# Kernel tuning notes

Hardware: AMD Instinct MI355X
Metric: run time of the kernel (lower is better)

Reference implementation:

```python
import math
import jax, jax.numpy as jnp
import numpy as np

D_MODEL, D_HEAD, N_HEADS, COND = 1024, 64, 16, 1024
BATCH, L_T, H_S, W_S = 2, 8, 16, 16
N_FREQS = D_HEAD // 8  # rotary freqs per axis; 3 axes -> rotates 3*D_HEAD/4 dims
EPS = 1e-6


def _ste(x, qx):
    # straight-through estimator: forward qx, backward identity
    return x + jax.lax.stop_gradient(qx - x)


def _weight_quant(w):
    # BitNet-1.58 ternary: per-tensor absmean scale, round to {-1,0,1}
    s = 1.0 / jnp.clip(jnp.mean(jnp.abs(w)), 1e-5)
    return jnp.clip(jnp.round(w * s), -1.0, 1.0) / s


def _act_quant(x):
    # per-token int8 absmax quant
    s = 127.0 / jnp.clip(jnp.max(jnp.abs(x), axis=-1, keepdims=True), 1e-5)
    return jnp.clip(jnp.round(x * s), -128.0, 127.0) / s


def bit_linear(x, w):
    return _ste(x, _act_quant(x)) @ _ste(w, _weight_quant(w)).T


def rms_norm(x, scale, eps=EPS):
    ms = jnp.mean(x * x, axis=-1, keepdims=True)
    return x * scale * jax.lax.rsqrt(ms + eps)


def apply_rotary_emb(x, theta):
    # rotate first 2*d dims of x (d = theta.shape[-1]); pass the rest through
    d = theta.shape[-1]
    x1, x2, x3 = x[..., :d], x[..., d:2 * d], x[..., 2 * d:]
    cos, sin = jnp.cos(theta), jnp.sin(theta)
    return jnp.concatenate([x1 * cos - x2 * sin, x2 * cos + x1 * sin, x3], axis=-1)


def make_freqs():
    # log-spaced pi..10*pi, distributed across heads (k-diffusion AxialRoPE init)
    log_min, log_max = math.log(math.pi), math.log(10.0 * math.pi)
    f = jnp.exp(jnp.linspace(log_min, log_max, N_HEADS * N_FREQS + 1)[:-1])
    return f.reshape(N_FREQS, N_HEADS).T.astype(jnp.float32)  # [n_heads, n_freqs]


def setup_inputs() -> dict:
    key = jax.random.key(0)
    ks = jax.random.split(key, 6)
    x = jax.random.normal(ks[0], (BATCH, L_T, H_S, W_S, D_MODEL), jnp.float32)
    pos = jax.random.uniform(ks[1], (BATCH, L_T, H_S, W_S, 3), jnp.float32) * 2.0 - 1.0
    cond = jax.random.normal(ks[2], (BATCH, COND), jnp.float32)
    norm_w = jax.random.normal(ks[3], (D_MODEL, COND), jnp.float32) * 0.02
    qkv_w = jax.random.normal(ks[4], (3 * D_MODEL, D_MODEL), jnp.float32) * 0.02
    out_w = jax.random.normal(ks[5], (D_MODEL, D_MODEL), jnp.float32) * 0.02
    scale = jnp.full((N_HEADS,), 10.0, jnp.float32)
    freqs = make_freqs()
    return dict(x=x, pos=pos, cond=cond, norm_w=norm_w, qkv_w=qkv_w,
                out_w=out_w, scale=scale, freqs=freqs)


def reference(x, pos, cond, norm_w, qkv_w, out_w, scale, freqs):
    n, l, h, w, d = x.shape
    L = l * h * w
    skip = x
    # AdaRMSNorm: scale = 1 + zero-init Linear(cond)
    ada = 1.0 + cond @ norm_w.T                      # [n, d]
    xn = rms_norm(x, ada[:, None, None, None, :])
    # BitLinear QKV projection
    qkv = bit_linear(xn.reshape(n, L, d), qkv_w)     # [n, L, 3d]
    qkv = qkv.reshape(n, L, 3, N_HEADS, D_HEAD).transpose(2, 0, 3, 1, 4)  # [3,n,nh,L,e]
    q, k, v = qkv[0], qkv[1], qkv[2]
    # cosine-sim rescale with learned per-head scale
    sqrt_s = jnp.sqrt(scale)[:, None, None]          # [nh,1,1]
    q = q * (sqrt_s * jax.lax.rsqrt(jnp.sum(q * q, -1, keepdims=True) + EPS))
    k = k * (sqrt_s * jax.lax.rsqrt(jnp.sum(k * k, -1, keepdims=True) + EPS))
    # axial RoPE over 3 axes
    p = pos.reshape(n, L, 3)
    theta = jnp.concatenate([p[..., None, a:a + 1] * freqs for a in range(3)], axis=-1)  # [n,L,nh,3*nf]
    theta = jnp.moveaxis(theta, -2, -3)              # [n,nh,L,3*nf]
    q = apply_rotary_emb(q, theta)
    k = apply_rotary_emb(k, theta)
    # SDPA with scale=1.0 (cosine-sim already scaled)
    attn = jax.nn.softmax(jnp.einsum('nhqe,nhke->nhqk', q, k), axis=-1)
    o = jnp.einsum('nhqk,nhke->nhqe', attn, v)       # [n,nh,L,e]
    o = o.transpose(0, 2, 1, 3).reshape(n, L, d)
    o = bit_linear(o, out_w).reshape(n, l, h, w, d)
    return o + skip
```

## Files before the change

kernel.cpp:

```cpp
#include <hip/hip_runtime.h>
#include <hip/hip_bf16.h>
#include <math.h>

typedef __attribute__((ext_vector_type(8))) short bf16x8;
typedef __attribute__((ext_vector_type(4))) short bf16x4;
typedef __attribute__((ext_vector_type(4))) float f32x4;
typedef __attribute__((ext_vector_type(16))) float f32x16;
typedef __attribute__((ext_vector_type(4))) unsigned u32x4;
typedef __attribute__((ext_vector_type(2))) unsigned u32x2;
typedef __attribute__((ext_vector_type(4))) int i32x4;

#define DEV static __device__ __forceinline__
#define LOG2E 1.4426950408889634f
#define INV2PI 0.15915494309189535f

DEV unsigned short f2bf(float f) {
  unsigned int u = __float_as_uint(f);
  u += 0x7FFFu + ((u >> 16) & 1u);
  return (unsigned short)(u >> 16);
}
DEV float bf2f(unsigned short h) { return __uint_as_float(((unsigned int)h) << 16); }
DEV unsigned cvtpk(float lo, float hi) {
  unsigned r;
  asm("v_cvt_pk_bf16_f32 %0, %1, %2" : "=v"(r) : "v"(lo), "v"(hi));
  return r;
}
DEV float exp2raw(float x) {
  float r;
  asm("v_exp_f32 %0, %1" : "=v"(r) : "v"(x));
  return r;
}
DEV float fract_raw(float x) { float r; asm("v_fract_f32 %0, %1" : "=v"(r) : "v"(x)); return r; }
DEV float sin_rev(float x)   { float r; asm("v_sin_f32 %0, %1"   : "=v"(r) : "v"(x)); return r; }
DEV float cos_rev(float x)   { float r; asm("v_cos_f32 %0, %1"   : "=v"(r) : "v"(x)); return r; }
DEV float wsum(float v) { for (int o = 32; o; o >>= 1) v += __shfl_xor(v, o); return v; }
DEV float wmaxr(float v) { for (int o = 32; o; o >>= 1) v = fmaxf(v, __shfl_xor(v, o)); return v; }

DEV void gload_lds16(const void* g, void* s) {
  __builtin_amdgcn_global_load_lds(
      (const __attribute__((address_space(1))) unsigned int*)g,
      (__attribute__((address_space(3))) unsigned int*)s, 16, 0, 0);
}

__global__ __launch_bounds__(256) void wrada_k(const float* __restrict__ qw,
                                               const float* __restrict__ ow,
                                               const float* __restrict__ cond,
                                               const float* __restrict__ nw,
                                               float* __restrict__ rowsum,
                                               float* __restrict__ ada) {
  if (blockIdx.x < 4096) {
    int row = blockIdx.x;
    const float* p = (row < 3072) ? (qw + (size_t)row * 1024)
                                  : (ow + (size_t)(row - 3072) * 1024);
    f32x4 v = *(const f32x4*)&p[threadIdx.x * 4];
    float s = fabsf(v[0]) + fabsf(v[1]) + fabsf(v[2]) + fabsf(v[3]);
    s = wsum(s);
    __shared__ float sh[4];
    if ((threadIdx.x & 63) == 0) sh[threadIdx.x >> 6] = s;
    __syncthreads();
    if (threadIdx.x == 0) rowsum[row] = sh[0] + sh[1] + sh[2] + sh[3];
  } else {
    int bid2 = blockIdx.x - 4096;
    int b = bid2 >> 8;
    int j = (bid2 & 255) * 4 + (threadIdx.x >> 6);
    int l = threadIdx.x & 63;
    const float* cp = cond + b * 1024;
    const float* wp = nw + (size_t)j * 1024;
    float s = 0.f;
    for (int c = l; c < 1024; c += 64) s += cp[c] * wp[c];
    s = wsum(s);
    if (l == 0) ada[b * 1024 + j] = 1.f + s;
  }
}

__global__ __launch_bounds__(256) void finalize_k(const float* __restrict__ rowsum,
                                                  float* __restrict__ scales) {
  float s1 = 0.f, s2 = 0.f;
  for (int i = threadIdx.x; i < 3072; i += 256) s1 += rowsum[i];
  for (int i = threadIdx.x; i < 1024; i += 256) s2 += rowsum[3072 + i];
  s1 = wsum(s1); s2 = wsum(s2);
  __shared__ float sh1[4], sh2[4];
  if ((threadIdx.x & 63) == 0) { sh1[threadIdx.x >> 6] = s1; sh2[threadIdx.x >> 6] = s2; }
  __syncthreads();
  if (threadIdx.x == 0) {
    float m1 = fmaxf((sh1[0] + sh1[1] + sh1[2] + sh1[3]) / (3072.f * 1024.f), 1e-5f);
    float m2 = fmaxf((sh2[0] + sh2[1] + sh2[2] + sh2[3]) / (1024.f * 1024.f), 1e-5f);
    scales[0] = m1; scales[1] = 1.f / m1;
    scales[2] = m2; scales[3] = 1.f / m2;
  }
}

__global__ __launch_bounds__(256) void wqrms_k(const float* __restrict__ qw,
                                               const float* __restrict__ ow,
                                               const float* __restrict__ scales,
                                               const float* __restrict__ x,
                                               const float* __restrict__ ada,
                                               signed char* __restrict__ Wq,
                                               signed char* __restrict__ Wo,
                                               signed char* __restrict__ Aq,
                                               float* __restrict__ ascale) {
  if (blockIdx.x < 4096) {
    int i0 = (blockIdx.x * 256 + threadIdx.x) * 4;
    if (i0 < 3072 * 1024) {
      f32x4 v = *(const f32x4*)&qw[i0];
      unsigned pk = 0;
      for (int j = 0; j < 4; j++) {
        int t = (int)fminf(fmaxf(rintf(v[j] * scales[1]), -1.f), 1.f);
        pk |= ((unsigned)t & 0xFFu) << (8 * j);
      }
      *(unsigned*)&Wq[i0] = pk;
    } else {
      int k = i0 - 3072 * 1024;
      f32x4 v = *(const f32x4*)&ow[k];
      unsigned pk = 0;
      for (int j = 0; j < 4; j++) {
        int t = (int)fminf(fmaxf(rintf(v[j] * scales[3]), -1.f), 1.f);
        pk |= ((unsigned)t & 0xFFu) << (8 * j);
      }
      *(unsigned*)&Wo[k] = pk;
    }
  } else {
    int row = blockIdx.x - 4096;
    int b = row >> 11;
    const float* xr = x + (size_t)row * 1024;
    const float* ar = ada + b * 1024;
    int t4 = threadIdx.x * 4;
    f32x4 v = *(const f32x4*)&xr[t4];
    float ss = v[0]*v[0] + v[1]*v[1] + v[2]*v[2] + v[3]*v[3];
    ss = wsum(ss);
    __shared__ float sh[4], sh2[4];
    if ((threadIdx.x & 63) == 0) sh[threadIdx.x >> 6] = ss;
    __syncthreads();
    float inv = rsqrtf((sh[0] + sh[1] + sh[2] + sh[3]) * (1.f / 1024.f) + 1e-6f);
    f32x4 a = *(const f32x4*)&ar[t4];
    float xn[4]; float mx = 0.f;
    for (int i = 0; i < 4; i++) { xn[i] = v[i] * a[i] * inv; mx = fmaxf(mx, fabsf(xn[i])); }
    mx = wmaxr(mx);
    if ((threadIdx.x & 63) == 0) sh2[threadIdx.x >> 6] = mx;
    __syncthreads();
    float rmax = fmaxf(fmaxf(sh2[0], sh2[1]), fmaxf(sh2[2], sh2[3]));
    float s = 127.f / fmaxf(rmax, 1e-5f);
    unsigned pk = 0;
    for (int i = 0; i < 4; i++) {
      int ai = (int)fminf(fmaxf(rintf(xn[i] * s), -128.f), 127.f);
      pk |= ((unsigned)ai & 0xFFu) << (8 * i);
    }
    *(unsigned*)&Aq[(size_t)row * 1024 + t4] = pk;
    if (threadIdx.x == 0) ascale[row] = 1.f / s;
  }
}

__global__ __launch_bounds__(256) void oquant_k(const unsigned short* __restrict__ Opart,
                                                const float* __restrict__ ms,
                                                signed char* __restrict__ Oq,
                                                float* __restrict__ oscale) {
  int row = blockIdx.x;
  int b = row >> 11, qrow = row & 2047;
  int t4 = threadIdx.x * 4;
  int h = t4 >> 6, e0 = t4 & 63;
  int bh = b * 16 + h;
  size_t i0 = (size_t)bh * 2048 + qrow;
  size_t i1 = (size_t)(32 + bh) * 2048 + qrow;
  float w = 1.f / (ms[i0] + ms[i1]);
  bf16x4 o0 = *(const bf16x4*)&Opart[i0 * 64 + e0];
  bf16x4 o1 = *(const bf16x4*)&Opart[i1 * 64 + e0];
  float v[4]; float mx = 0.f;
  for (int i = 0; i < 4; i++) {
    v[i] = (bf2f((unsigned short)o0[i]) + bf2f((unsigned short)o1[i])) * w;
    mx = fmaxf(mx, fabsf(v[i]));
  }
  mx = wmaxr(mx);
  __shared__ float sh[4];
  if ((threadIdx.x & 63) == 0) sh[threadIdx.x >> 6] = mx;
  __syncthreads();
  float rmax = fmaxf(fmaxf(sh[0], sh[1]), fmaxf(sh[2], sh[3]));
  float s = 127.f / fmaxf(rmax, 1e-5f);
  float is = 1.f / s;
  unsigned pk = 0;
  for (int i = 0; i < 4; i++) {
    int ai = (int)fminf(fmaxf(rintf(v[i] * s), -128.f), 127.f);
    pk |= ((unsigned)ai & 0xFFu) << (8 * i);
  }
  *(unsigned*)&Oq[(size_t)row * 1024 + t4] = pk;
  if (threadIdx.x == 0) oscale[row] = is;
}

__global__ __launch_bounds__(256, 3) void gemm_i8(const signed char* __restrict__ A8,
                                                  const signed char* __restrict__ B8,
                                                  int N, int K, int nwg, int mode,
                                                  const float* __restrict__ rowsc,
                                                  const float* __restrict__ wscp,
                                                  const float* __restrict__ skip,
                                                  float* __restrict__ outF,
                                                  unsigned short* __restrict__ outB) {
  __shared__ signed char As[2][128 * 64];
  __shared__ signed char Bs[2][128 * 64];
  int bid = blockIdx.x;
  int wg = (bid % 8) * (nwg >> 3) + (bid >> 3);
  int bx = wg & 31, by = wg >> 5;
  int tid = threadIdx.x;
  int w = tid >> 6, l = tid & 63;
  int q = l & 15, g = l >> 4;
  int tm = bx * 128, tn = by * 128;
  int wr = w >> 1, wc = w & 1;
  float wsc = wscp[0];
  i32x4 acc[4][4];
  i32x4 zero = {0, 0, 0, 0};
#pragma unroll
  for (int m = 0; m < 4; m++)
#pragma unroll
    for (int n = 0; n < 4; n++) acc[m][n] = zero;
  int s0 = w * 64 + l, s1 = 256 + s0;
  int r0 = s0 >> 2, p0 = s0 & 3, gs0 = p0 ^ ((r0 >> 1) & 3);
  int r1 = s1 >> 2, p1 = s1 & 3, gs1 = p1 ^ ((r1 >> 1) & 3);
  const signed char* Ag0 = A8 + (size_t)(tm + r0) * K + gs0 * 16;
  const signed char* Ag1 = A8 + (size_t)(tm + r1) * K + gs1 * 16;
  const signed char* Bg0 = B8 + (size_t)(tn + r0) * K + gs0 * 16;
  const signed char* Bg1 = B8 + (size_t)(tn + r1) * K + gs1 * 16;
  int posq = ((q >> 1) & 3);

  auto stage = [&](int buf, int k0) {
    gload_lds16(Ag0 + k0, &As[buf][w * 1024]);
    gload_lds16(Ag1 + k0, &As[buf][4096 + w * 1024]);
    gload_lds16(Bg0 + k0, &Bs[buf][w * 1024]);
    gload_lds16(Bg1 + k0, &Bs[buf][4096 + w * 1024]);
  };

  stage(0, 0);
  __syncthreads();
  int cur = 0;
  for (int k0 = 0; k0 < K; k0 += 64) {
    if (k0 + 64 < K) stage(cur ^ 1, k0 + 64);
    int pg = (g ^ posq) * 16;
    i32x4 af[4], bfr[4];
#pragma unroll
    for (int m = 0; m < 4; m++)
      af[m] = *(const i32x4*)&As[cur][(wr * 64 + m * 16 + q) * 64 + pg];
#pragma unroll
    for (int n = 0; n < 4; n++)
      bfr[n] = *(const i32x4*)&Bs[cur][(wc * 64 + n * 16 + q) * 64 + pg];
#pragma unroll
    for (int m = 0; m < 4; m++)
#pragma unroll
      for (int n = 0; n < 4; n++)
        acc[m][n] = __builtin_amdgcn_mfma_i32_16x16x64_i8(af[m], bfr[n], acc[m][n], 0, 0, 0);
    __syncthreads();
    cur ^= 1;
  }
#pragma unroll
  for (int m = 0; m < 4; m++) {
#pragma unroll
    for (int r = 0; r < 4; r++) {
      int row = tm + wr * 64 + m * 16 + g * 4 + r;
      float dq = rowsc[row] * wsc;
#pragma unroll
      for (int n = 0; n < 4; n++) {
        int col = tn + wc * 64 + n * 16 + q;
        float vv = (float)acc[m][n][r] * dq;
        if (mode == 0) outB[(size_t)row * N + col] = f2bf(vv);
        else { size_t idx = (size_t)row * N + col; outF[idx] = vv + skip[idx]; }
      }
    }
  }
}

__global__ __launch_bounds__(256) void prep_k(const unsigned short* __restrict__ qkv,
                                              const float* __restrict__ pos,
                                              const float* __restrict__ scale,
                                              const float* __restrict__ freqs,
                                              unsigned short* __restrict__ Qo,
                                              unsigned short* __restrict__ Ko,
                                              unsigned short* __restrict__ VT) {
  __shared__ unsigned short tile[64][72];
  int tid = threadIdx.x;
  if (blockIdx.x < 4096) {
    int t = blockIdx.x & 2047, b = blockIdx.x >> 11;
    int half = tid >> 7;
    int i = tid & 127;
    int h = i >> 3, j = i & 7;
    int lane = tid & 63;
    const unsigned short* src =
        qkv + ((size_t)(b * 2048 + t)) * 3072 + half * 1024 + h * 64 + j * 8;
    bf16x8 vv = *(const bf16x8*)src;
    float f[8]; float ss = 0.f;
#pragma unroll
    for (int m = 0; m < 8; m++) { f[m] = bf2f((unsigned short)vv[m]); ss += f[m] * f[m]; }
    ss += __shfl_xor(ss, 1);
    ss += __shfl_xor(ss, 2);
    ss += __shfl_xor(ss, 4);
    float fac = sqrtf(scale[h]) * rsqrtf(ss + 1e-6f);
#pragma unroll
    for (int m = 0; m < 8; m++) f[m] *= fac;
    int plane = (j < 3) ? lane + 3 : ((j < 6) ? lane - 3 : lane);
    float p[8];
#pragma unroll
    for (int m = 0; m < 8; m++) p[m] = __shfl(f[m], plane);
    float outv[8];
    if (j < 6) {
      int a = (j < 3) ? j : j - 3;
      float sgn = (j < 3) ? -1.f : 1.f;
      float pth = pos[((size_t)(b * 2048 + t)) * 3 + a];
      f32x4 fr0 = *(const f32x4*)&freqs[h * 8];
      f32x4 fr1 = *(const f32x4*)&freqs[h * 8 + 4];
#pragma unroll
      for (int m = 0; m < 8; m++) {
        float frq = (m < 4) ? fr0[m] : fr1[m - 4];
        float rev = fract_raw(pth * frq * INV2PI);
        float sn = sin_rev(rev), cs = cos_rev(rev);
        outv[m] = f[m] * cs + sgn * p[m] * sn;
      }
    } else {
#pragma unroll
      for (int m = 0; m < 8; m++) outv[m] = f[m];
    }
    bf16x8 o;
    size_t oi = ((size_t)((b * 16 + h) * 2048 + t)) * 64 + j * 8;
    if (half == 0) {
#pragma unroll
      for (int m = 0; m < 8; m++) o[m] = (short)f2bf(outv[m] * LOG2E);
      *(bf16x8*)(Qo + oi) = o;
    } else {
#pragma unroll
      for (int m = 0; m < 8; m++) o[m] = (short)f2bf(outv[m]);
      *(bf16x8*)(Ko + oi) = o;
    }
  } else {
    int bid2 = blockIdx.x - 4096;
    int tt = bid2 & 31, bh = bid2 >> 5;
    int b = bh >> 4, h = bh & 15;
    for (int ro = 0; ro < 2; ro++) {
      int r = ro * 32 + (tid >> 3);
      int c = (tid & 7) * 8;
      *(bf16x8*)&tile[r][c] =
          *(const bf16x8*)(qkv + ((size_t)(b * 2048 + tt * 64 + r)) * 3072 + 2048 + h * 64 + c);
    }
    __syncthreads();
    int e = tid >> 2;
    int tc = (tid & 3) * 16;
    bf16x8 o0, o1;
#pragma unroll
    for (int i = 0; i < 4; i++) {
      o0[i]     = (short)tile[tc + i][e];
      o0[4 + i] = (short)tile[tc + 8 + i][e];
      o1[i]     = (short)tile[tc + 4 + i][e];
      o1[4 + i] = (short)tile[tc + 12 + i][e];
    }
    unsigned short* dst = VT + ((size_t)(bh * 64 + e)) * 2048 + tt * 64 + tc;
    *(bf16x8*)dst = o0;
    *(bf16x8*)(dst + 8) = o1;
  }
}

__global__ __launch_bounds__(512, 4) void attn_k(const unsigned short* __restrict__ Q,
                                                 const unsigned short* __restrict__ K,
                                                 const unsigned short* __restrict__ VT,
                                                 unsigned short* __restrict__ Opart,
                                                 float* __restrict__ ms) {
  __shared__ unsigned short Ks[2][128 * 64];
  __shared__ unsigned short Vs[2][64 * 128];
  const float M0 = 15.0f;
  int tid = threadIdx.x;
  int w = tid >> 6, l = tid & 63;
  int q = l & 31, hi = l >> 5;
  int bid = blockIdx.x;
  int sbh = (bid >> 6) * 8 + (bid & 7);
  int qg = (bid >> 3) & 7;
  int split = sbh >> 5, bh = sbh & 31;
  int qrow0 = qg * 256 + w * 32;
  const unsigned short* Kbase = K + (size_t)bh * 2048 * 64 + (size_t)split * 1024 * 64;
  const unsigned short* Vbase = VT + (size_t)bh * 64 * 2048 + split * 1024;

  bf16x8 qa[4];
#pragma unroll
  for (int s = 0; s < 4; s++)
    qa[s] = *(const bf16x8*)(Q + ((size_t)bh * 2048 + qrow0 + q) * 64 + s * 16 + hi * 8);

  int koff0[4], koff1[4], voff0[4], voff1[4];
#pragma unroll
  for (int se = 0; se < 4; se++) {
    int gk = se * 2 + hi;
    koff0[se] = q * 64 + ((gk ^ (q & 7)) * 8);
    koff1[se] = (32 + q) * 64 + ((gk ^ (q & 7)) * 8);
    voff0[se] = q * 128 + ((gk ^ (q & 7)) * 8);
    voff1[se] = (32 + q) * 128 + ((gk ^ (q & 7)) * 8);
  }

  int slA = tid, slB = 512 + tid;
  int krA = slA >> 3, kgA = (slA & 7) ^ (krA & 7);
  int krB = slB >> 3, kgB = (slB & 7) ^ (krB & 7);
  int vrA = slA >> 4, vgA = (slA & 15) ^ (vrA & 7);
  int vrB = slB >> 4, vgB = (slB & 15) ^ (vrB & 7);
  const unsigned short* KgA = Kbase + (size_t)krA * 64 + kgA * 8;
  const unsigned short* KgB = Kbase + (size_t)krB * 64 + kgB * 8;
  const unsigned short* VgA = Vbase + (size_t)vrA * 2048 + vgA * 8;
  const unsigned short* VgB = Vbase + (size_t)vrB * 2048 + vgB * 8;

  f32x16 acc0, acc1, fz;
  for (int i = 0; i < 16; i++) { acc0[i] = 0.f; acc1[i] = 0.f; fz[i] = 0.f; }
  float sum = 0.f;

  auto stage = [&](int buf, int kt) {
    gload_lds16(KgA + (size_t)kt * 64, &Ks[buf][(w * 64) * 8]);
    gload_lds16(KgB + (size_t)kt * 64, &Ks[buf][(512 + w * 64) * 8]);
    gload_lds16(VgA + kt, &Vs[buf][(w * 64) * 8]);
    gload_lds16(VgB + kt, &Vs[buf][(512 + w * 64) * 8]);
  };

  stage(0, 0);
  __syncthreads();
  int cur = 0;
  for (int it = 0; it < 8; it++) {
    if (it < 7) stage(cur ^ 1, (it + 1) * 128);
    const unsigned short* Ksc = Ks[cur];
    const unsigned short* Vsc = Vs[cur];
#pragma unroll
    for (int ss = 0; ss < 2; ss++) {
      int kro = ss * 4096;
      int vco = ss * 64;
      bf16x8 ka0 = *(const bf16x8*)&Ksc[kro + koff0[0]];
      bf16x8 ka1 = *(const bf16x8*)&Ksc[kro + koff1[0]];
      __builtin_amdgcn_s_setprio(1);
      f32x16 s0 = __builtin_amdgcn_mfma_f32_32x32x16_bf16(ka0, qa[0], fz, 0, 0, 0);
      f32x16 s1 = __builtin_amdgcn_mfma_f32_32x32x16_bf16(ka1, qa[0], fz, 0, 0, 0);
#pragma unroll
      for (int se = 1; se < 4; se++) {
        ka0 = *(const bf16x8*)&Ksc[kro + koff0[se]];
        ka1 = *(const bf16x8*)&Ksc[kro + koff1[se]];
        s0 = __builtin_amdgcn_mfma_f32_32x32x16_bf16(ka0, qa[se], s0, 0, 0, 0);
        s1 = __builtin_amdgcn_mfma_f32_32x32x16_bf16(ka1, qa[se], s1, 0, 0, 0);
      }
      __builtin_amdgcn_s_setprio(0);

      bf16x8 pf[4];
#pragma unroll
      for (int n = 0; n < 4; n++) {
        int o = (n & 1) * 8;
        u32x4 t;
#pragma unroll
        for (int j = 0; j < 4; j++) {
          float a = (n < 2) ? s0[o + 2 * j] : s1[o + 2 * j];
          float b = (n < 2) ? s0[o + 2 * j + 1] : s1[o + 2 * j + 1];
          float e0 = exp2raw(a - M0);
          float e1 = exp2raw(b - M0);
          sum += e0 + e1;
          t[j] = cvtpk(e0, e1);
        }
        pf[n] = __builtin_bit_cast(bf16x8, t);
      }

      __builtin_amdgcn_s_setprio(1);
#pragma unroll
      for (int n = 0; n < 4; n++) {
        bf16x8 va0 = *(const bf16x8*)&Vsc[vco + voff0[n]];
        bf16x8 va1 = *(const bf16x8*)&Vsc[vco + voff1[n]];
        acc0 = __builtin_amdgcn_mfma_f32_32x32x16_bf16(va0, pf[n], acc0, 0, 0, 0);
        acc1 = __builtin_amdgcn_mfma_f32_32x32x16_bf16(va1, pf[n], acc1, 0, 0, 0);
      }
      __builtin_amdgcn_s_setprio(0);
    }
    __syncthreads();
    cur ^= 1;
  }

  sum += __shfl_xor(sum, 32);
  size_t prow = (size_t)(split * 32 + bh) * 2048 + qrow0 + q;
  unsigned short* Op = Opart + prow * 64;
#pragma unroll
  for (int et = 0; et < 2; et++) {
    const f32x16& a = et ? acc1 : acc0;
#pragma unroll
    for (int qd = 0; qd < 4; qd++) {
      int e0 = et * 32 + 4 * hi + qd * 8;
      u32x2 t;
      t[0] = cvtpk(a[qd * 4 + 0], a[qd * 4 + 1]);
      t[1] = cvtpk(a[qd * 4 + 2], a[qd * 4 + 3]);
      *(bf16x4*)&Op[e0] = __builtin_bit_cast(bf16x4, t);
    }
  }
  if (hi == 0) ms[prow] = sum;
}

extern "C" void kernel_launch(void* const* d_in, const int* in_sizes, int n_in,
                              void* d_out, int out_size, void* d_ws, size_t ws_size,
                              hipStream_t stream) {
  const float* x      = (const float*)d_in[0];
  const float* pos    = (const float*)d_in[1];
  const float* cond   = (const float*)d_in[2];
  const float* norm_w = (const float*)d_in[3];
  const float* qkv_w  = (const float*)d_in[4];
  const float* out_w  = (const float*)d_in[5];
  const float* scale  = (const float*)d_in[6];
  const float* freqs  = (const float*)d_in[7];
  float* out = (float*)d_out;
  char* ws = (char*)d_ws;

  const size_t o_ada    = 0;
  const size_t o_rowsum = 8192;
  const size_t o_scales = 24576;
  const size_t o_ascale = 24832;
  const size_t o_oscale = 41216;
  const size_t o_Wq8    = 57600;
  const size_t o_Wo8    = o_Wq8 + 3145728;
  const size_t o_AqQ    = o_Wo8 + 1048576;
  const size_t o_qkv    = o_AqQ + 8388608;
  const size_t o_K      = o_qkv + 25165824;
  const size_t o_VT     = o_K + 8388608;

  float* ada            = (float*)(ws + o_ada);
  float* rowsum         = (float*)(ws + o_rowsum);
  float* scales         = (float*)(ws + o_scales);
  float* ascale         = (float*)(ws + o_ascale);
  float* oscale         = (float*)(ws + o_oscale);
  signed char* Wq8      = (signed char*)(ws + o_Wq8);
  signed char* Wo8      = (signed char*)(ws + o_Wo8);
  signed char* Aq8      = (signed char*)(ws + o_AqQ);
  unsigned short* Qb    = (unsigned short*)(ws + o_AqQ);
  unsigned short* qkv   = (unsigned short*)(ws + o_qkv);
  unsigned short* Opart = (unsigned short*)(ws + o_qkv);
  float* msb            = (float*)(ws + o_qkv + 2ull*32*2048*64*2);
  unsigned short* Kb    = (unsigned short*)(ws + o_K);
  signed char* Oq8      = (signed char*)(ws + o_K);
  unsigned short* VT    = (unsigned short*)(ws + o_VT);

  wrada_k<<<4608, 256, 0, stream>>>(qkv_w, out_w, cond, norm_w, rowsum, ada);
  finalize_k<<<1, 256, 0, stream>>>(rowsum, scales);
  wqrms_k<<<8192, 256, 0, stream>>>(qkv_w, out_w, scales, x, ada, Wq8, Wo8, Aq8, ascale);
  gemm_i8<<<768, 256, 0, stream>>>(Aq8, Wq8, 3072, 1024, 768, 0, ascale, &scales[0],
                                   nullptr, nullptr, qkv);
  prep_k<<<5120, 256, 0, stream>>>(qkv, pos, scale, freqs, Qb, Kb, VT);
  attn_k<<<512, 512, 0, stream>>>(Qb, Kb, VT, Opart, msb);
  oquant_k<<<4096, 256, 0, stream>>>(Opart, msb, Oq8, oscale);
  gemm_i8<<<256, 256, 0, stream>>>(Oq8, Wo8, 1024, 1024, 256, 1, oscale, &scales[2],
                                   x, out, nullptr);
}
```

Measured before the change: 141.3 us.

## Fuse V transpose into QKV GEMM epilogue, shrink prep kernel to Q/K

The QKV int8 GEMM epilogue now writes the V columns straight into the transposed VT layout, with a token permutation that matches the attention kernel's expected ordering. Only Q/K are stored to a narrower 2048-wide intermediate. This removes the transpose block branch from prep_k, which cuts a kernel stage's global read/write of V and some blocks. The cost is that the GEMM epilogue now does strided 8-byte scattered stores for V, which may coalesce poorly.

```diff
diff --git a/kernel.cpp b/kernel.cpp
--- a/kernel.cpp
+++ b/kernel.cpp
@@ -192,7 +192,8 @@
                                                   const float* __restrict__ wscp,
                                                   const float* __restrict__ skip,
                                                   float* __restrict__ outF,
-                                                  unsigned short* __restrict__ outB) {
+                                                  unsigned short* __restrict__ outB,
+                                                  unsigned short* __restrict__ vtout) {
   __shared__ signed char As[2][128 * 64];
   __shared__ signed char Bs[2][128 * 64];
   int bid = blockIdx.x;
@@ -247,107 +248,109 @@
     __syncthreads();
     cur ^= 1;
   }
-#pragma unroll
-  for (int m = 0; m < 4; m++) {
-#pragma unroll
-    for (int r = 0; r < 4; r++) {
-      int row = tm + wr * 64 + m * 16 + g * 4 + r;
-      float dq = rowsc[row] * wsc;
+  if (mode == 0) {
+#pragma unroll
+    for (int m = 0; m < 4; m++) {
+      int row0 = tm + wr * 64 + m * 16 + g * 4;
 #pragma unroll
       for (int n = 0; n < 4; n++) {
         int col = tn + wc * 64 + n * 16 + q;
-        float vv = (float)acc[m][n][r] * dq;
-        if (mode == 0) outB[(size_t)row * N + col] = f2bf(vv);
-        else { size_t idx = (size_t)row * N + col; outF[idx] = vv + skip[idx]; }
-      }
-    }
-  }
-}
-
-__global__ __launch_bounds__(256) void prep_k(const unsigned short* __restrict__ qkv,
+        if (col < 2048) {
+#pragma unroll
+          for (int r = 0; r < 4; r++) {
+            int row = row0 + r;
+            float vv = (float)acc[m][n][r] * (rowsc[row] * wsc);
+            outB[(size_t)row * 2048 + col] = f2bf(vv);
+          }
+        } else {
+          int h = (col - 2048) >> 6, e = col & 63;
+          int t0 = row0 & 2047, b = row0 >> 11;
+          int tp0 = (t0 & ~12) | ((t0 & 4) << 1) | ((t0 & 8) >> 1);
+          bf16x4 u;
+#pragma unroll
+          for (int r = 0; r < 4; r++) {
+            int row = row0 + r;
+            float vv = (float)acc[m][n][r] * (rowsc[row] * wsc);
+            u[r] = (short)f2bf(vv);
+          }
+          *(bf16x4*)&vtout[((size_t)((b * 16 + h) * 64 + e)) * 2048 + tp0] = u;
+        }
+      }
+    }
+  } else {
+#pragma unroll
+    for (int m = 0; m < 4; m++) {
+#pragma unroll
+      for (int r = 0; r < 4; r++) {
+        int row = tm + wr * 64 + m * 16 + g * 4 + r;
+        float dq = rowsc[row] * wsc;
+#pragma unroll
+        for (int n = 0; n < 4; n++) {
+          int col = tn + wc * 64 + n * 16 + q;
+          size_t idx = (size_t)row * N + col;
+          outF[idx] = (float)acc[m][n][r] * dq + skip[idx];
+        }
+      }
+    }
+  }
+}
+
+__global__ __launch_bounds__(256) void prep_k(const unsigned short* __restrict__ qk,
                                               const float* __restrict__ pos,
                                               const float* __restrict__ scale,
                                               const float* __restrict__ freqs,
                                               unsigned short* __restrict__ Qo,
-                                              unsigned short* __restrict__ Ko,
-                                              unsigned short* __restrict__ VT) {
-  __shared__ unsigned short tile[64][72];
+                                              unsigned short* __restrict__ Ko) {
   int tid = threadIdx.x;
-  if (blockIdx.x < 4096) {
-    int t = blockIdx.x & 2047, b = blockIdx.x >> 11;
-    int half = tid >> 7;
-    int i = tid & 127;
-    int h = i >> 3, j = i & 7;
-    int lane = tid & 63;
-    const unsigned short* src =
-        qkv + ((size_t)(b * 2048 + t)) * 3072 + half * 1024 + h * 64 + j * 8;
-    bf16x8 vv = *(const bf16x8*)src;
-    float f[8]; float ss = 0.f;
-#pragma unroll
-    for (int m = 0; m < 8; m++) { f[m] = bf2f((unsigned short)vv[m]); ss += f[m] * f[m]; }
-    ss += __shfl_xor(ss, 1);
-    ss += __shfl_xor(ss, 2);
-    ss += __shfl_xor(ss, 4);
-    float fac = sqrtf(scale[h]) * rsqrtf(ss + 1e-6f);
-#pragma unroll
-    for (int m = 0; m < 8; m++) f[m] *= fac;
-    int plane = (j < 3) ? lane + 3 : ((j < 6) ? lane - 3 : lane);
-    float p[8];
-#pragma unroll
-    for (int m = 0; m < 8; m++) p[m] = __shfl(f[m], plane);
-    float outv[8];
-    if (j < 6) {
-      int a = (j < 3) ? j : j - 3;
-      float sgn = (j < 3) ? -1.f : 1.f;
-      float pth = pos[((size_t)(b * 2048 + t)) * 3 + a];
-      f32x4 fr0 = *(const f32x4*)&freqs[h * 8];
-      f32x4 fr1 = *(const f32x4*)&freqs[h * 8 + 4];
-#pragma unroll
-      for (int m = 0; m < 8; m++) {
-        float frq = (m < 4) ? fr0[m] : fr1[m - 4];
-        float rev = fract_raw(pth * frq * INV2PI);
-        float sn = sin_rev(rev), cs = cos_rev(rev);
-        outv[m] = f[m] * cs + sgn * p[m] * sn;
-      }
-    } else {
-#pragma unroll
-      for (int m = 0; m < 8; m++) outv[m] = f[m];
-    }
-    bf16x8 o;
-    size_t oi = ((size_t)((b * 16 + h) * 2048 + t)) * 64 + j * 8;
-    if (half == 0) {
-#pragma unroll
-      for (int m = 0; m < 8; m++) o[m] = (short)f2bf(outv[m] * LOG2E);
-      *(bf16x8*)(Qo + oi) = o;
-    } else {
-#pragma unroll
-      for (int m = 0; m < 8; m++) o[m] = (short)f2bf(outv[m]);
-      *(bf16x8*)(Ko + oi) = o;
+  int t = blockIdx.x & 2047, b = blockIdx.x >> 11;
+  int half = tid >> 7;
+  int i = tid & 127;
+  int h = i >> 3, j = i & 7;
+  int lane = tid & 63;
+  const unsigned short* src =
+      qk + ((size_t)(b * 2048 + t)) * 2048 + half * 1024 + h * 64 + j * 8;
+  bf16x8 vv = *(const bf16x8*)src;
+  float f[8]; float ss = 0.f;
+#pragma unroll
+  for (int m = 0; m < 8; m++) { f[m] = bf2f((unsigned short)vv[m]); ss += f[m] * f[m]; }
+  ss += __shfl_xor(ss, 1);
+  ss += __shfl_xor(ss, 2);
+  ss += __shfl_xor(ss, 4);
+  float fac = sqrtf(scale[h]) * rsqrtf(ss + 1e-6f);
+#pragma unroll
+  for (int m = 0; m < 8; m++) f[m] *= fac;
+  int plane = (j < 3) ? lane + 3 : ((j < 6) ? lane - 3 : lane);
+  float p[8];
+#pragma unroll
+  for (int m = 0; m < 8; m++) p[m] = __shfl(f[m], plane);
+  float outv[8];
+  if (j < 6) {
+    int a = (j < 3) ? j : j - 3;
+    float sgn = (j < 3) ? -1.f : 1.f;
+    float pth = pos[((size_t)(b * 2048 + t)) * 3 + a];
+    f32x4 fr0 = *(const f32x4*)&freqs[h * 8];
+    f32x4 fr1 = *(const f32x4*)&freqs[h * 8 + 4];
+#pragma unroll
+    for (int m = 0; m < 8; m++) {
+      float frq = (m < 4) ? fr0[m] : fr1[m - 4];
+      float rev = fract_raw(pth * frq * INV2PI);
+      float sn = sin_rev(rev), cs = cos_rev(rev);
+      outv[m] = f[m] * cs + sgn * p[m] * sn;
     }
   } else {
-    int bid2 = blockIdx.x - 4096;
-    int tt = bid2 & 31, bh = bid2 >> 5;
-    int b = bh >> 4, h = bh & 15;
-    for (int ro = 0; ro < 2; ro++) {
-      int r = ro * 32 + (tid >> 3);
-      int c = (tid & 7) * 8;
-      *(bf16x8*)&tile[r][c] =
-          *(const bf16x8*)(qkv + ((size_t)(b * 2048 + tt * 64 + r)) * 3072 + 2048 + h * 64 + c);
-    }
-    __syncthreads();
-    int e = tid >> 2;
-    int tc = (tid & 3) * 16;
-    bf16x8 o0, o1;
-#pragma unroll
-    for (int i = 0; i < 4; i++) {
-      o0[i]     = (short)tile[tc + i][e];
-      o0[4 + i] = (short)tile[tc + 8 + i][e];
-      o1[i]     = (short)tile[tc + 4 + i][e];
-      o1[4 + i] = (short)tile[tc + 12 + i][e];
-    }
-    unsigned short* dst = VT + ((size_t)(bh * 64 + e)) * 2048 + tt * 64 + tc;
-    *(bf16x8*)dst = o0;
-    *(bf16x8*)(dst + 8) = o1;
+#pragma unroll
+    for (int m = 0; m < 8; m++) outv[m] = f[m];
+  }
+  bf16x8 o;
+  size_t oi = ((size_t)((b * 16 + h) * 2048 + t)) * 64 + j * 8;
+  if (half == 0) {
+#pragma unroll
+    for (int m = 0; m < 8; m++) o[m] = (short)f2bf(outv[m] * LOG2E);
+    *(bf16x8*)(Qo + oi) = o;
+  } else {
+#pragma unroll
+    for (int m = 0; m < 8; m++) o[m] = (short)f2bf(outv[m]);
+    *(bf16x8*)(Ko + oi) = o;
   }
 }
 
@@ -515,7 +518,7 @@
   signed char* Wo8      = (signed char*)(ws + o_Wo8);
   signed char* Aq8      = (signed char*)(ws + o_AqQ);
   unsigned short* Qb    = (unsigned short*)(ws + o_AqQ);
-  unsigned short* qkv   = (unsigned short*)(ws + o_qkv);
+  unsigned short* qk    = (unsigned short*)(ws + o_qkv);
   unsigned short* Opart = (unsigned short*)(ws + o_qkv);
   float* msb            = (float*)(ws + o_qkv + 2ull*32*2048*64*2);
   unsigned short* Kb    = (unsigned short*)(ws + o_K);
@@ -526,10 +529,10 @@
   finalize_k<<<1, 256, 0, stream>>>(rowsum, scales);
   wqrms_k<<<8192, 256, 0, stream>>>(qkv_w, out_w, scales, x, ada, Wq8, Wo8, Aq8, ascale);
   gemm_i8<<<768, 256, 0, stream>>>(Aq8, Wq8, 3072, 1024, 768, 0, ascale, &scales[0],
-                                   nullptr, nullptr, qkv);
-  prep_k<<<5120, 256, 0, stream>>>(qkv, pos, scale, freqs, Qb, Kb, VT);
+                                   nullptr, nullptr, qk, VT);
+  prep_k<<<4096, 256, 0, stream>>>(qk, pos, scale, freqs, Qb, Kb);
   attn_k<<<512, 512, 0, stream>>>(Qb, Kb, VT, Opart, msb);
   oquant_k<<<4096, 256, 0, stream>>>(Opart, msb, Oq8, oscale);
   gemm_i8<<<256, 256, 0, stream>>>(Oq8, Wo8, 1024, 1024, 256, 1, oscale, &scales[2],
-                                   x, out, nullptr);
-}
+                                   x, out, nullptr, nullptr);
+}
```

New measurement: 134.4 us. -4.9%, faster.
